# Kernel tuning notes

Hardware: AMD Instinct MI355X
Metric: run time of the kernel (lower is better)

Reference implementation:

```python
import jax, jax.numpy as jnp
import numpy as np

Q_DIM = 2048
HEADS = 16
HEAD_DIM = 128
INNER = HEADS * HEAD_DIM          # 2048
MLP_HID = int(Q_DIM * 4.0)        # 8192
MLP_MULT = 2
EPS = 1e-05
B, S = 2, 2048


def setup_inputs() -> dict:
    key = jax.random.key(0)
    ks = jax.random.split(key, 4)
    hidden_states = jax.random.normal(ks[0], (B, S, Q_DIM), dtype=jnp.float32)
    # interleaved RoPE tables: cos/sin of shape [S, HEAD_DIM]
    half = HEAD_DIM // 2
    freqs = 1.0 / (10000.0 ** (np.arange(half, dtype=np.float64) / half))
    ang = np.outer(np.arange(S, dtype=np.float64), freqs)      # [S, half]
    ang = np.repeat(ang, 2, axis=-1)                            # [S, HEAD_DIM]
    rope_cos = jnp.asarray(np.cos(ang), dtype=jnp.float32)
    rope_sin = jnp.asarray(np.sin(ang), dtype=jnp.float32)
    fused_out = 3 * INNER + MLP_HID * MLP_MULT                  # 22528
    W_qkv_mlp = jax.random.normal(ks[1], (Q_DIM, fused_out), dtype=jnp.float32) * (Q_DIM ** -0.5)
    norm_q_w = jnp.ones((HEAD_DIM,), dtype=jnp.float32)
    norm_k_w = jnp.ones((HEAD_DIM,), dtype=jnp.float32)
    W_out = jax.random.normal(ks[2], (INNER + MLP_HID, Q_DIM), dtype=jnp.float32) * ((INNER + MLP_HID) ** -0.5)
    b_out = jnp.zeros((Q_DIM,), dtype=jnp.float32)
    return {"hidden_states": hidden_states, "rope_cos": rope_cos, "rope_sin": rope_sin,
            "W_qkv_mlp": W_qkv_mlp, "norm_q_w": norm_q_w, "norm_k_w": norm_k_w,
            "W_out": W_out, "b_out": b_out}


def _rms_norm(x, w):
    # RMSNorm over the last (head_dim) axis
    return x * jax.lax.rsqrt(jnp.mean(x * x, axis=-1, keepdims=True) + EPS) * w


def _apply_rope(x, cos, sin):
    # x: [B, S, H, D]; interleaved rotate-half (diffusers real-rope convention)
    xr = x.reshape(*x.shape[:-1], HEAD_DIM // 2, 2)
    rot = jnp.stack([-xr[..., 1], xr[..., 0]], axis=-1).reshape(x.shape)
    return x * cos[None, :, None, :] + rot * sin[None, :, None, :]


def reference(hidden_states, rope_cos, rope_sin, W_qkv_mlp, norm_q_w, norm_k_w, W_out, b_out):
    b, s, _ = hidden_states.shape
    proj = hidden_states @ W_qkv_mlp                              # [B,S,22528]
    qkv, mlp_h = jnp.split(proj, [3 * INNER], axis=-1)
    q, k, v = jnp.split(qkv, 3, axis=-1)
    q = q.reshape(b, s, HEADS, HEAD_DIM)
    k = k.reshape(b, s, HEADS, HEAD_DIM)
    v = v.reshape(b, s, HEADS, HEAD_DIM)
    q = _rms_norm(q, norm_q_w)
    k = _rms_norm(k, norm_k_w)
    q = _apply_rope(q, rope_cos, rope_sin)
    k = _apply_rope(k, rope_cos, rope_sin)
    scale = HEAD_DIM ** -0.5
    scores = jnp.einsum('bqhd,bkhd->bhqk', q, k) * scale          # [B,H,S,S]
    attn = jax.nn.softmax(scores, axis=-1)
    out_attn = jnp.einsum('bhqk,bkhd->bqhd', attn, v).reshape(b, s, INNER)
    m1, m2 = jnp.split(mlp_h, 2, axis=-1)                         # SwiGLU
    mlp_out = jax.nn.silu(m1) * m2                                # [B,S,MLP_HID]
    cat = jnp.concatenate([out_attn, mlp_out], axis=-1)           # [B,S,INNER+MLP_HID]
    return cat @ W_out + b_out
```

## Files before the change

kernel.cpp:

```cpp
#include <hip/hip_runtime.h>

typedef unsigned short u16;
typedef unsigned int u32;
typedef __bf16 bf16x8 __attribute__((ext_vector_type(8)));
typedef float f32x4 __attribute__((ext_vector_type(4)));

#define MFMA16(a, b, c) __builtin_amdgcn_mfma_f32_16x16x32_bf16((a), (b), (c), 0, 0, 0)

#define S_LEN 2048
#define D_HEAD 128
#define NHEADS 16
#define NBH 32
#define QDIM 2048
#define NPROJ 22528
#define NQKV 6144
#define NMLP 16384
#define NCAT 10240
#define MROWS 4096

#define BARRIER() __builtin_amdgcn_s_barrier()
#define WAITVM0() asm volatile("s_waitcnt vmcnt(0)" ::: "memory")

__device__ __forceinline__ float bf2f(u16 u) { return __uint_as_float(((u32)u) << 16); }
__device__ __forceinline__ u16 f2bf(float f) {
  u32 u = __float_as_uint(f);
  return (u16)((u + 0x7FFFu + ((u >> 16) & 1u)) >> 16);
}
__device__ __forceinline__ void gld16(const void* g, void* l) {
  __builtin_amdgcn_global_load_lds((__attribute__((address_space(1))) void*)(g),
                                   (__attribute__((address_space(3))) void*)(l), 16, 0, 0);
}

__global__ __launch_bounds__(256) void f32_to_bf16(const float* __restrict__ in,
                                                   u16* __restrict__ out) {
  const u32 i = blockIdx.x * 256 + threadIdx.x;
  const float4 v = ((const float4*)in)[i];
  uint2 o;
  o.x = (u32)f2bf(v.x) | ((u32)f2bf(v.y) << 16);
  o.y = (u32)f2bf(v.z) | ((u32)f2bf(v.w) << 16);
  ((uint2*)out)[i] = o;
}

template <int REMAP>
__global__ __launch_bounds__(256) void transpose_f32_bf16(const float* __restrict__ in,
                                                          u16* __restrict__ out, int R, int C) {
  __shared__ u16 tile[64][65];
  const int tx = threadIdx.x & 63;
  const int ty = threadIdx.x >> 6;
  const int c0 = blockIdx.x * 64;
  const int r0 = blockIdx.y * 64;
#pragma unroll
  for (int it = 0; it < 16; ++it) {
    const int rr = ty * 16 + it;
    tile[rr][tx] = f2bf(in[(size_t)(r0 + rr) * C + c0 + tx]);
  }
  __syncthreads();
#pragma unroll
  for (int it = 0; it < 16; ++it) {
    const int rr = ty * 16 + it;
    int orow = c0 + rr;
    if (REMAP && orow >= NQKV) {
      const int c = orow - NQKV;
      const int f = c & 8191;
      const int sel = c >> 13;
      orow = NQKV + (((f >> 4) << 5) | (sel << 4) | (f & 15));
    }
    out[(size_t)orow * R + r0 + tx] = tile[tx][rr];
  }
}

__global__ __launch_bounds__(256) void transpose_bf16_b(const u16* __restrict__ in,
                                                        u16* __restrict__ out, int R, int C) {
  __shared__ u16 tile[64][65];
  const int z = blockIdx.z;
  in += (size_t)z * R * C;
  out += (size_t)z * R * C;
  const int tx = threadIdx.x & 63;
  const int ty = threadIdx.x >> 6;
  const int c0 = blockIdx.x * 64;
  const int r0 = blockIdx.y * 64;
#pragma unroll
  for (int it = 0; it < 16; ++it) {
    const int rr = ty * 16 + it;
    tile[rr][tx] = in[(size_t)(r0 + rr) * C + c0 + tx];
  }
  __syncthreads();
#pragma unroll
  for (int it = 0; it < 16; ++it) {
    const int rr = ty * 16 + it;
    out[(size_t)(c0 + rr) * R + r0 + tx] = tile[tx][rr];
  }
}

template <int OUTMODE>
__global__ __launch_bounds__(256, 2) void gemm_bt(const u16* __restrict__ A,
                                                  const u16* __restrict__ Bt,
                                                  void* __restrict__ Cvoid,
                                                  const float* __restrict__ bias, int N, int K) {
  __shared__ u16 As[128 * 64];
  __shared__ u16 Bs[128 * 64];
  const int t = threadIdx.x;
  const int l = t & 63;
  const int w = t >> 6;
  const int lr = l & 15;
  const int lg = l >> 4;
  const int m0 = blockIdx.y * 128;
  const int n0 = blockIdx.x * 128;
  const int wm = (w >> 1) * 64;
  const int wn = (w & 1) * 64;

  f32x4 acc[4][4] = {};
  const int obase = w * 1024 + l * 16;

  for (int k0 = 0; k0 < K; k0 += 64) {
#pragma unroll
    for (int rnd = 0; rnd < 4; ++rnd) {
      const int o = obase + rnd * 4096;
      const int row = o >> 7;
      const int g = (o & 127) >> 4;
      const int gs = g ^ (row & 7);
      gld16(A + (size_t)(m0 + row) * K + k0 + gs * 8, &As[rnd * 2048 + w * 512]);
      gld16(Bt + (size_t)(n0 + row) * K + k0 + gs * 8, &Bs[rnd * 2048 + w * 512]);
    }
    __syncthreads();

    bf16x8 af[4][2], bfr[4][2];
#pragma unroll
    for (int i = 0; i < 4; ++i) {
#pragma unroll
      for (int kc = 0; kc < 2; ++kc) {
        const int ra = wm + i * 16 + lr;
        af[i][kc] = *(const bf16x8*)&As[ra * 64 + (((kc * 4 + lg) ^ (ra & 7)) * 8)];
        const int rb = wn + i * 16 + lr;
        bfr[i][kc] = *(const bf16x8*)&Bs[rb * 64 + (((kc * 4 + lg) ^ (rb & 7)) * 8)];
      }
    }
#pragma unroll
    for (int kc = 0; kc < 2; ++kc)
#pragma unroll
      for (int i = 0; i < 4; ++i)
#pragma unroll
        for (int j = 0; j < 4; ++j)
          acc[i][j] = MFMA16(af[i][kc], bfr[j][kc], acc[i][j]);
    __syncthreads();
  }

  if (OUTMODE == 1) {
    float* C = (float*)Cvoid;
#pragma unroll
    for (int i = 0; i < 4; ++i)
#pragma unroll
      for (int j = 0; j < 4; ++j)
#pragma unroll
        for (int r = 0; r < 4; ++r) {
          const int row = m0 + wm + i * 16 + lg * 4 + r;
          const int col = n0 + wn + j * 16 + lr;
          C[(size_t)row * N + col] = acc[i][j][r] + bias[col];
        }
  } else if (OUTMODE == 0) {
    u16* C = (u16*)Cvoid;
#pragma unroll
    for (int i = 0; i < 4; ++i)
#pragma unroll
      for (int j = 0; j < 4; ++j)
#pragma unroll
        for (int r = 0; r < 4; ++r) {
          const int row = m0 + wm + i * 16 + lg * 4 + r;
          const int col = n0 + wn + j * 16 + lr;
          C[(size_t)row * N + col] = f2bf(acc[i][j][r]);
        }
  } else {
    u16* C = (u16*)Cvoid;
#pragma unroll
    for (int i = 0; i < 4; ++i)
#pragma unroll
      for (int jj = 0; jj < 2; ++jj)
#pragma unroll
        for (int r = 0; r < 4; ++r) {
          const int row = m0 + wm + i * 16 + lg * 4 + r;
          const float a1 = acc[i][2 * jj][r];
          const float a2 = acc[i][2 * jj + 1][r];
          const float fz = a1 / (1.f + __expf(-a1)) * a2;
          const int col = ((n0 + wn) >> 1) + jj * 16 + lr;
          C[(size_t)row * N + col] = f2bf(fz);
        }
  }
}

__global__ __launch_bounds__(256, 2) void gemm_qkv(const u16* __restrict__ A,
                                                   const u16* __restrict__ Bt,
                                                   const float* __restrict__ cosT,
                                                   const float* __restrict__ sinT,
                                                   const float* __restrict__ wq,
                                                   const float* __restrict__ wk,
                                                   u16* __restrict__ Qb, u16* __restrict__ Kb,
                                                   u16* __restrict__ Vb, int K) {
  __shared__ u16 As[128 * 64];
  __shared__ u16 Bs[128 * 64];
  __shared__ float redbuf[2][128];
  const int t = threadIdx.x;
  const int l = t & 63;
  const int w = t >> 6;
  const int lr = l & 15;
  const int lg = l >> 4;
  const int m0 = blockIdx.y * 128;
  const int n0 = blockIdx.x * 128;
  const int wm = (w >> 1) * 64;
  const int wn = (w & 1) * 64;

  f32x4 acc[4][4] = {};
  const int obase = w * 1024 + l * 16;

  for (int k0 = 0; k0 < K; k0 += 64) {
#pragma unroll
    for (int rnd = 0; rnd < 4; ++rnd) {
      const int o = obase + rnd * 4096;
      const int row = o >> 7;
      const int g = (o & 127) >> 4;
      const int gs = g ^ (row & 7);
      gld16(A + (size_t)(m0 + row) * K + k0 + gs * 8, &As[rnd * 2048 + w * 512]);
      gld16(Bt + (size_t)(n0 + row) * K + k0 + gs * 8, &Bs[rnd * 2048 + w * 512]);
    }
    __syncthreads();

    bf16x8 af[4][2], bfr[4][2];
#pragma unroll
    for (int i = 0; i < 4; ++i) {
#pragma unroll
      for (int kc = 0; kc < 2; ++kc) {
        const int ra = wm + i * 16 + lr;
        af[i][kc] = *(const bf16x8*)&As[ra * 64 + (((kc * 4 + lg) ^ (ra & 7)) * 8)];
        const int rb = wn + i * 16 + lr;
        bfr[i][kc] = *(const bf16x8*)&Bs[rb * 64 + (((kc * 4 + lg) ^ (rb & 7)) * 8)];
      }
    }
#pragma unroll
    for (int kc = 0; kc < 2; ++kc)
#pragma unroll
      for (int i = 0; i < 4; ++i)
#pragma unroll
        for (int j = 0; j < 4; ++j)
          acc[i][j] = MFMA16(af[i][kc], bfr[j][kc], acc[i][j]);
    __syncthreads();
  }

  const int type = n0 >> 11;
  const int h = (n0 >> 7) & 15;
  u16* dst = (type == 0) ? Qb : (type == 1) ? Kb : Vb;

  if (type == 2) {
#pragma unroll
    for (int i = 0; i < 4; ++i)
#pragma unroll
      for (int j = 0; j < 4; ++j)
#pragma unroll
        for (int r = 0; r < 4; ++r) {
          const int row = m0 + wm + i * 16 + lg * 4 + r;
          const int s = row & 2047, b = row >> 11;
          const int col = wn + j * 16 + lr;
          dst[((size_t)(b * 16 + h) * S_LEN + s) * 128 + col] = f2bf(acc[i][j][r]);
        }
    return;
  }

  float ssum[4][4];
#pragma unroll
  for (int i = 0; i < 4; ++i)
#pragma unroll
    for (int r = 0; r < 4; ++r) {
      float p = acc[i][0][r] * acc[i][0][r] + acc[i][1][r] * acc[i][1][r] +
                acc[i][2][r] * acc[i][2][r] + acc[i][3][r] * acc[i][3][r];
      p += __shfl_xor(p, 1);
      p += __shfl_xor(p, 2);
      p += __shfl_xor(p, 4);
      p += __shfl_xor(p, 8);
      ssum[i][r] = p;
    }
  if (lr == 0) {
#pragma unroll
    for (int i = 0; i < 4; ++i)
#pragma unroll
      for (int r = 0; r < 4; ++r) redbuf[wn >> 6][wm + i * 16 + lg * 4 + r] = ssum[i][r];
  }
  __syncthreads();

  const float* wgt = type ? wk : wq;
  const float sc = type ? 1.0f : 0.08838834764831845f;
#pragma unroll
  for (int i = 0; i < 4; ++i)
#pragma unroll
    for (int r = 0; r < 4; ++r) {
      const int lrow = wm + i * 16 + lg * 4 + r;
      const float tot = redbuf[0][lrow] + redbuf[1][lrow];
      const float rsq = rsqrtf(tot * (1.0f / 128.0f) + 1e-5f) * sc;
      const int row = m0 + lrow;
      const int s = row & 2047, b = row >> 11;
      const size_t rbase = ((size_t)(b * 16 + h) * S_LEN + s) * 128;
#pragma unroll
      for (int j = 0; j < 4; ++j) {
        const int col = wn + j * 16 + lr;
        const float xn = acc[i][j][r] * rsq * wgt[col];
        const float pr = __shfl_xor(xn, 1);
        const float c = cosT[s * 128 + col];
        const float sn = sinT[s * 128 + col];
        const float val = (col & 1) ? (xn * c + pr * sn) : (xn * c - pr * sn);
        dst[rbase + col] = f2bf(val);
      }
    }
}

__global__ __launch_bounds__(256, 2) void attn_fwd(const u16* __restrict__ Qb,
                                                   const u16* __restrict__ Kb,
                                                   const u16* __restrict__ Vt,
                                                   u16* __restrict__ Cat) {
  __shared__ u16 Ks[2][64 * 128];
  __shared__ u16 Vs[2][128 * 64];
  __shared__ u16 Ps[4][32 * 64];

  const int t = threadIdx.x;
  const int l = t & 63;
  const int w = t >> 6;
  const int lr = l & 15;
  const int lg = l >> 4;
  const int qt = blockIdx.x;
  const int bh = blockIdx.y;
  const int b = bh >> 4;
  const int h = bh & 15;
  const int q0 = qt * 128 + w * 32;
  const int obase = w * 1024 + l * 16;

  const size_t kbase = (size_t)bh * S_LEN * 128;
  const size_t vbase = (size_t)bh * 128 * S_LEN;

  bf16x8 qf[2][4];
#pragma unroll
  for (int im = 0; im < 2; ++im)
#pragma unroll
    for (int kc = 0; kc < 4; ++kc)
      qf[im][kc] =
          *(const bf16x8*)&Qb[((size_t)bh * S_LEN + q0 + im * 16 + lr) * 128 + kc * 32 + lg * 8];

  f32x4 oacc[2][8] = {};
  float lrun[2][4] = {};

  u16* P = Ps[w];

  auto stageKV = [&](int buf, int kt2) {
    const int kk0 = kt2 * 64;
#pragma unroll
    for (int rnd = 0; rnd < 4; ++rnd) {
      const int o = obase + rnd * 4096;
      {
        const int key = o >> 8;
        const int g = (o & 255) >> 4;
        const int gs = g ^ (key & 7);
        gld16(Kb + kbase + (size_t)(kk0 + key) * 128 + gs * 8,
              &Ks[buf][rnd * 2048 + w * 512]);
      }
      {
        const int d = o >> 7;
        const int g = (o & 127) >> 4;
        const int gs = g ^ (d & 7);
        gld16(Vt + vbase + (size_t)d * S_LEN + kk0 + gs * 8,
              &Vs[buf][rnd * 2048 + w * 512]);
      }
    }
  };

  stageKV(0, 0);
  WAITVM0();
  BARRIER();

  int cur = 0;
  for (int kt = 0; kt < 32; ++kt) {
    if (kt + 1 < 32) stageKV(cur ^ 1, kt + 1);

    const u16* Kc = &Ks[cur][0];
    const u16* Vc = &Vs[cur][0];

    f32x4 sf[2][4] = {};
    __builtin_amdgcn_s_setprio(1);
#pragma unroll
    for (int j = 0; j < 4; ++j) {
      const int kr = j * 16 + lr;
      bf16x8 kf[4];
#pragma unroll
      for (int kc = 0; kc < 4; ++kc)
        kf[kc] = *(const bf16x8*)&Kc[kr * 128 + (((kc * 4 + lg) ^ (kr & 7)) * 8)];
#pragma unroll
      for (int kc = 0; kc < 4; ++kc)
#pragma unroll
        for (int im = 0; im < 2; ++im)
          sf[im][j] = MFMA16(qf[im][kc], kf[kc], sf[im][j]);
    }
    __builtin_amdgcn_s_setprio(0);

#pragma unroll
    for (int im = 0; im < 2; ++im) {
#pragma unroll
      for (int r = 0; r < 4; ++r) {
        float psum = 0.f;
#pragma unroll
        for (int j = 0; j < 4; ++j) {
          const float pv = __expf(sf[im][j][r]);
          sf[im][j][r] = pv;
          psum += pv;
        }
        psum += __shfl_xor(psum, 1);
        psum += __shfl_xor(psum, 2);
        psum += __shfl_xor(psum, 4);
        psum += __shfl_xor(psum, 8);
        lrun[im][r] += psum;
      }
    }

#pragma unroll
    for (int im = 0; im < 2; ++im)
#pragma unroll
      for (int j = 0; j < 4; ++j)
#pragma unroll
        for (int r = 0; r < 4; ++r) {
          const int q = im * 16 + lg * 4 + r;
          const int key = j * 16 + lr;
          const int g = key >> 3;
          P[q * 64 + ((g ^ (q & 7)) * 8) + (key & 7)] = f2bf(sf[im][j][r]);
        }

    __builtin_amdgcn_s_setprio(1);
#pragma unroll
    for (int kc = 0; kc < 2; ++kc) {
      bf16x8 pa[2];
#pragma unroll
      for (int im = 0; im < 2; ++im) {
        const int q = im * 16 + lr;
        pa[im] = *(const bf16x8*)&P[q * 64 + (((kc * 4 + lg) ^ (q & 7)) * 8)];
      }
#pragma unroll
      for (int df = 0; df < 8; ++df) {
        const int d = df * 16 + lr;
        const bf16x8 vb = *(const bf16x8*)&Vc[d * 64 + (((kc * 4 + lg) ^ (d & 7)) * 8)];
#pragma unroll
        for (int im = 0; im < 2; ++im) oacc[im][df] = MFMA16(pa[im], vb, oacc[im][df]);
      }
    }
    __builtin_amdgcn_s_setprio(0);

    WAITVM0();
    BARRIER();
    cur ^= 1;
  }

#pragma unroll
  for (int im = 0; im < 2; ++im)
#pragma unroll
    for (int r = 0; r < 4; ++r) {
      const float inv = 1.0f / lrun[im][r];
      const int row = b * S_LEN + q0 + im * 16 + lg * 4 + r;
#pragma unroll
      for (int df = 0; df < 8; ++df) {
        const int col = h * 128 + df * 16 + lr;
        Cat[(size_t)row * NCAT + col] = f2bf(oacc[im][df][r] * inv);
      }
    }
}

extern "C" void kernel_launch(void* const* d_in, const int* in_sizes, int n_in, void* d_out,
                              int out_size, void* d_ws, size_t ws_size, hipStream_t stream) {
  (void)in_sizes; (void)n_in; (void)out_size; (void)ws_size;
  const float* hs = (const float*)d_in[0];
  const float* rcos = (const float*)d_in[1];
  const float* rsin = (const float*)d_in[2];
  const float* Wqkv = (const float*)d_in[3];
  const float* wq = (const float*)d_in[4];
  const float* wk = (const float*)d_in[5];
  const float* Wout = (const float*)d_in[6];
  const float* bout = (const float*)d_in[7];
  float* out = (float*)d_out;

  char* ws = (char*)d_ws;
  size_t off = 0;
  auto nxt = [&](size_t bytes) {
    char* p = ws + off;
    off += (bytes + 255) & ~(size_t)255;
    return p;
  };
  u16* Xb = (u16*)nxt((size_t)MROWS * QDIM * 2);
  u16* Wqkvt = (u16*)nxt((size_t)NPROJ * QDIM * 2);
  u16* Woutt = (u16*)nxt((size_t)QDIM * NCAT * 2);
  u16* Qb = (u16*)nxt((size_t)NBH * S_LEN * D_HEAD * 2);
  u16* Kb = (u16*)nxt((size_t)NBH * S_LEN * D_HEAD * 2);
  u16* Vb = (u16*)nxt((size_t)NBH * S_LEN * D_HEAD * 2);
  u16* Vt = (u16*)nxt((size_t)NBH * S_LEN * D_HEAD * 2);
  u16* Cat = (u16*)nxt((size_t)MROWS * NCAT * 2);

  f32_to_bf16<<<(MROWS * QDIM / 4) / 256, 256, 0, stream>>>(hs, Xb);
  transpose_f32_bf16<1><<<dim3(NPROJ / 64, QDIM / 64), 256, 0, stream>>>(Wqkv, Wqkvt, QDIM,
                                                                         NPROJ);
  transpose_f32_bf16<0><<<dim3(QDIM / 64, NCAT / 64), 256, 0, stream>>>(Wout, Woutt, NCAT, QDIM);

  gemm_qkv<<<dim3(NQKV / 128, MROWS / 128), 256, 0, stream>>>(Xb, Wqkvt, rcos, rsin, wq, wk,
                                                              Qb, Kb, Vb, QDIM);
  gemm_bt<2><<<dim3(NMLP / 128, MROWS / 128), 256, 0, stream>>>(
      Xb, Wqkvt + (size_t)NQKV * QDIM, Cat + QDIM, nullptr, NCAT, QDIM);

  transpose_bf16_b<<<dim3(D_HEAD / 64, S_LEN / 64, NBH), 256, 0, stream>>>(Vb, Vt, S_LEN, D_HEAD);

  attn_fwd<<<dim3(S_LEN / 128, NBH), 256, 0, stream>>>(Qb, Kb, Vt, Cat);

  gemm_bt<1><<<dim3(QDIM / 128, MROWS / 128), 256, 0, stream>>>(Cat, Woutt, out, bout, QDIM,
                                                                NCAT);
}
```

Before: 777.5 us.

## Merge QKV and SwiGLU projection GEMMs, use exp2 softmax, swizzle attention blocks

```diff
diff --git a/kernel.cpp b/kernel.cpp
--- a/kernel.cpp
+++ b/kernel.cpp
@@ -92,7 +92,7 @@
   }
 }
 
-template <int OUTMODE>
+template <int OUTF32>
 __global__ __launch_bounds__(256, 2) void gemm_bt(const u16* __restrict__ A,
                                                   const u16* __restrict__ Bt,
                                                   void* __restrict__ Cvoid,
@@ -145,7 +145,7 @@
     __syncthreads();
   }
 
-  if (OUTMODE == 1) {
+  if (OUTF32) {
     float* C = (float*)Cvoid;
 #pragma unroll
     for (int i = 0; i < 4; ++i)
@@ -157,7 +157,7 @@
           const int col = n0 + wn + j * 16 + lr;
           C[(size_t)row * N + col] = acc[i][j][r] + bias[col];
         }
-  } else if (OUTMODE == 0) {
+  } else {
     u16* C = (u16*)Cvoid;
 #pragma unroll
     for (int i = 0; i < 4; ++i)
@@ -169,32 +169,18 @@
           const int col = n0 + wn + j * 16 + lr;
           C[(size_t)row * N + col] = f2bf(acc[i][j][r]);
         }
-  } else {
-    u16* C = (u16*)Cvoid;
-#pragma unroll
-    for (int i = 0; i < 4; ++i)
-#pragma unroll
-      for (int jj = 0; jj < 2; ++jj)
-#pragma unroll
-        for (int r = 0; r < 4; ++r) {
-          const int row = m0 + wm + i * 16 + lg * 4 + r;
-          const float a1 = acc[i][2 * jj][r];
-          const float a2 = acc[i][2 * jj + 1][r];
-          const float fz = a1 / (1.f + __expf(-a1)) * a2;
-          const int col = ((n0 + wn) >> 1) + jj * 16 + lr;
-          C[(size_t)row * N + col] = f2bf(fz);
-        }
-  }
-}
-
-__global__ __launch_bounds__(256, 2) void gemm_qkv(const u16* __restrict__ A,
-                                                   const u16* __restrict__ Bt,
-                                                   const float* __restrict__ cosT,
-                                                   const float* __restrict__ sinT,
-                                                   const float* __restrict__ wq,
-                                                   const float* __restrict__ wk,
-                                                   u16* __restrict__ Qb, u16* __restrict__ Kb,
-                                                   u16* __restrict__ Vb, int K) {
+  }
+}
+
+__global__ __launch_bounds__(256, 2) void gemm_proj(const u16* __restrict__ A,
+                                                    const u16* __restrict__ Bt,
+                                                    const float* __restrict__ cosT,
+                                                    const float* __restrict__ sinT,
+                                                    const float* __restrict__ wq,
+                                                    const float* __restrict__ wk,
+                                                    u16* __restrict__ Qb, u16* __restrict__ Kb,
+                                                    u16* __restrict__ Vb, u16* __restrict__ Cat,
+                                                    int K) {
   __shared__ u16 As[128 * 64];
   __shared__ u16 Bs[128 * 64];
   __shared__ float redbuf[2][128];
@@ -244,6 +230,24 @@
     __syncthreads();
   }
 
+  if (n0 >= NQKV) {
+    const int nm = n0 - NQKV;
+#pragma unroll
+    for (int i = 0; i < 4; ++i)
+#pragma unroll
+      for (int jj = 0; jj < 2; ++jj)
+#pragma unroll
+        for (int r = 0; r < 4; ++r) {
+          const int row = m0 + wm + i * 16 + lg * 4 + r;
+          const float a1 = acc[i][2 * jj][r];
+          const float a2 = acc[i][2 * jj + 1][r];
+          const float fz = a1 / (1.f + __expf(-a1)) * a2;
+          const int col = QDIM + ((nm + wn) >> 1) + jj * 16 + lr;
+          Cat[(size_t)row * NCAT + col] = f2bf(fz);
+        }
+    return;
+  }
+
   const int type = n0 >> 11;
   const int h = (n0 >> 7) & 15;
   u16* dst = (type == 0) ? Qb : (type == 1) ? Kb : Vb;
@@ -285,7 +289,7 @@
   __syncthreads();
 
   const float* wgt = type ? wk : wq;
-  const float sc = type ? 1.0f : 0.08838834764831845f;
+  const float sc = type ? 1.0f : 0.12751744f;
 #pragma unroll
   for (int i = 0; i < 4; ++i)
 #pragma unroll
@@ -322,8 +326,9 @@
   const int w = t >> 6;
   const int lr = l & 15;
   const int lg = l >> 4;
-  const int qt = blockIdx.x;
-  const int bh = blockIdx.y;
+  const int swz = (blockIdx.x & 7) * 64 + (blockIdx.x >> 3);
+  const int qt = swz & 15;
+  const int bh = swz >> 4;
   const int b = bh >> 4;
   const int h = bh & 15;
   const int q0 = qt * 128 + w * 32;
@@ -396,23 +401,18 @@
     __builtin_amdgcn_s_setprio(0);
 
 #pragma unroll
-    for (int im = 0; im < 2; ++im) {
+    for (int im = 0; im < 2; ++im)
 #pragma unroll
       for (int r = 0; r < 4; ++r) {
         float psum = 0.f;
 #pragma unroll
         for (int j = 0; j < 4; ++j) {
-          const float pv = __expf(sf[im][j][r]);
+          const float pv = exp2f(sf[im][j][r]);
           sf[im][j][r] = pv;
           psum += pv;
         }
-        psum += __shfl_xor(psum, 1);
-        psum += __shfl_xor(psum, 2);
-        psum += __shfl_xor(psum, 4);
-        psum += __shfl_xor(psum, 8);
         lrun[im][r] += psum;
       }
-    }
 
 #pragma unroll
     for (int im = 0; im < 2; ++im)
@@ -454,7 +454,12 @@
   for (int im = 0; im < 2; ++im)
 #pragma unroll
     for (int r = 0; r < 4; ++r) {
-      const float inv = 1.0f / lrun[im][r];
+      float tot = lrun[im][r];
+      tot += __shfl_xor(tot, 1);
+      tot += __shfl_xor(tot, 2);
+      tot += __shfl_xor(tot, 4);
+      tot += __shfl_xor(tot, 8);
+      const float inv = 1.0f / tot;
       const int row = b * S_LEN + q0 + im * 16 + lg * 4 + r;
 #pragma unroll
       for (int df = 0; df < 8; ++df) {
@@ -498,14 +503,12 @@
                                                                          NPROJ);
   transpose_f32_bf16<0><<<dim3(QDIM / 64, NCAT / 64), 256, 0, stream>>>(Wout, Woutt, NCAT, QDIM);
 
-  gemm_qkv<<<dim3(NQKV / 128, MROWS / 128), 256, 0, stream>>>(Xb, Wqkvt, rcos, rsin, wq, wk,
-                                                              Qb, Kb, Vb, QDIM);
-  gemm_bt<2><<<dim3(NMLP / 128, MROWS / 128), 256, 0, stream>>>(
-      Xb, Wqkvt + (size_t)NQKV * QDIM, Cat + QDIM, nullptr, NCAT, QDIM);
+  gemm_proj<<<dim3(NPROJ / 128, MROWS / 128), 256, 0, stream>>>(Xb, Wqkvt, rcos, rsin, wq, wk,
+                                                                Qb, Kb, Vb, Cat, QDIM);
 
   transpose_bf16_b<<<dim3(D_HEAD / 64, S_LEN / 64, NBH), 256, 0, stream>>>(Vb, Vt, S_LEN, D_HEAD);
 
-  attn_fwd<<<dim3(S_LEN / 128, NBH), 256, 0, stream>>>(Qb, Kb, Vt, Cat);
+  attn_fwd<<<S_LEN / 128 * NBH, 256, 0, stream>>>(Qb, Kb, Vt, Cat);
 
   gemm_bt<1><<<dim3(QDIM / 128, MROWS / 128), 256, 0, stream>>>(Cat, Woutt, out, bout, QDIM,
                                                                 NCAT);
```

New measurement: 812.9 us. 4.6% more time.
